# Performance work log

Measured on AMD Instinct MI355X. Metric: run time of the kernel, lower is better.

The kernel has to match this reference:

```python
import jax, jax.numpy as jnp
import numpy as np

N_NODES = 40000
N_EDGES = 640000
IN, HID, OUT = 128, 256, 47


def setup_inputs() -> dict:
    key = jax.random.key(0)
    ks = jax.random.split(key, 8)
    x = jax.random.normal(ks[0], (N_NODES, IN), dtype=jnp.float32)
    # PyTorch Linear(fan_in, fan_out): store as [fan_in, fan_out] for y = h @ W + b
    W1 = jax.random.normal(ks[1], (2 * IN, HID), dtype=jnp.float32) / np.sqrt(2 * IN)
    b1 = jnp.zeros((HID,), jnp.float32)
    W2 = jax.random.normal(ks[2], (2 * HID, HID), dtype=jnp.float32) / np.sqrt(2 * HID)
    b2 = jnp.zeros((HID,), jnp.float32)
    W3 = jax.random.normal(ks[3], (2 * HID, OUT), dtype=jnp.float32) / np.sqrt(2 * HID)
    b3 = jnp.zeros((OUT,), jnp.float32)
    src = jax.random.randint(ks[4], (N_EDGES,), 0, N_NODES, dtype=jnp.int64 if jax.config.jax_enable_x64 else jnp.int32)
    dst = jax.random.randint(ks[5], (N_EDGES,), 0, N_NODES, dtype=jnp.int64 if jax.config.jax_enable_x64 else jnp.int32)
    return {"x": x, "W1": W1, "b1": b1, "W2": W2, "b2": b2, "W3": W3, "b3": b3,
            "src": src, "dst": dst}


def _sage_layer(h, src, dst, W, b):
    # copy_u -> mean: gather src features, scatter-sum into dst, divide by in-degree
    msum = jax.ops.segment_sum(h[src], dst, num_segments=N_NODES)  # [N, d]
    deg = jax.ops.segment_sum(jnp.ones_like(dst, dtype=h.dtype), dst, num_segments=N_NODES)
    mean = msum / jnp.maximum(deg, 1.0)[:, None]  # zero-degree nodes get 0 (DGL mean convention)
    cat = jnp.concatenate([h, mean], axis=1)      # [N, 2d]
    return cat @ W + b


def reference(x, W1, b1, W2, b2, W3, b3, src, dst):
    # dropout is identity in eval mode
    h = jax.nn.relu(_sage_layer(x, src, dst, W1, b1))
    h = jax.nn.relu(_sage_layer(h, src, dst, W2, b2))
    return _sage_layer(h, src, dst, W3, b3)
```

## Files before the change

kernel.cpp:

```cpp
#include <hip/hip_runtime.h>

#define NNODES 40000
#define NEDGES 640000
#define DIN 128
#define DHID 256
#define DOUT 47
#define NCNT 40960
#define NPART (NCNT / 256)

typedef __attribute__((ext_vector_type(8))) short short8;
typedef __attribute__((ext_vector_type(4))) float f32x4;

__device__ inline float bf2f(unsigned short u) {
    union { unsigned int i; float f; } c; c.i = ((unsigned int)u) << 16; return c.f;
}
__device__ inline unsigned short f2bf(float f) {
    union { float f; unsigned int i; } c; c.f = f;
    unsigned int x = c.i;
    x += 0x7fff + ((x >> 16) & 1);
    return (unsigned short)(x >> 16);
}

__global__ void hist_kernel(const int* __restrict__ dst, int* __restrict__ cnt) {
    int t = blockIdx.x * blockDim.x + threadIdx.x;
    if (t < NEDGES) atomicAdd(&cnt[dst[t]], 1);
}

__global__ void part_kernel(const int* __restrict__ cnt, int* __restrict__ part) {
    int b = blockIdx.x, t = threadIdx.x;
    int v = cnt[b * 256 + t];
#pragma unroll
    for (int off = 32; off > 0; off >>= 1) v += __shfl_down(v, off);
    __shared__ int ws[4];
    if ((t & 63) == 0) ws[t >> 6] = v;
    __syncthreads();
    if (t == 0) part[b] = ws[0] + ws[1] + ws[2] + ws[3];
}

__global__ void scanpart_kernel(const int* __restrict__ part, int* __restrict__ partoff) {
    __shared__ int sh[256];
    int t = threadIdx.x;
    int v = (t < NPART) ? part[t] : 0;
    sh[t] = v;
    __syncthreads();
    for (int off = 1; off < 256; off <<= 1) {
        int add = (t >= off) ? sh[t - off] : 0;
        __syncthreads();
        sh[t] += add;
        __syncthreads();
    }
    if (t < NPART) partoff[t] = sh[t] - v;
}

__global__ void writeptr_kernel(const int* __restrict__ cnt, const int* __restrict__ partoff,
                                int* __restrict__ rowptr) {
    __shared__ int sh[256];
    int b = blockIdx.x, t = threadIdx.x;
    int idx = b * 256 + t;
    int v = cnt[idx];
    sh[t] = v;
    __syncthreads();
    for (int off = 1; off < 256; off <<= 1) {
        int add = (t >= off) ? sh[t - off] : 0;
        __syncthreads();
        sh[t] += add;
        __syncthreads();
    }
    rowptr[idx] = partoff[b] + sh[t] - v;
}

__global__ void fill_kernel(const int* __restrict__ src, const int* __restrict__ dst,
                            const int* __restrict__ rowptr, int* __restrict__ fill,
                            unsigned short* __restrict__ eidx) {
    int e = blockIdx.x * blockDim.x + threadIdx.x;
    if (e < NEDGES) {
        int d = dst[e];
        int pos = rowptr[d] + atomicAdd(&fill[d], 1);
        eidx[pos] = (unsigned short)src[e];
    }
}

__global__ void f32_to_bf16x4_kernel(const float4* __restrict__ in, ushort4* __restrict__ out, int n4) {
    int t = blockIdx.x * blockDim.x + threadIdx.x;
    if (t < n4) {
        float4 v = in[t];
        ushort4 r;
        r.x = f2bf(v.x); r.y = f2bf(v.y); r.z = f2bf(v.z); r.w = f2bf(v.w);
        out[t] = r;
    }
}

__global__ void conv_wt_kernel(const float* __restrict__ W, unsigned short* __restrict__ Wt, int K, int N) {
    int t = blockIdx.x * blockDim.x + threadIdx.x;
    if (t < K * N) {
        int k = t / N, n = t - k * N;
        Wt[(size_t)n * K + k] = f2bf(W[t]);
    }
}

__global__ void conv_wt3_kernel(const float* __restrict__ W3, unsigned short* __restrict__ Wt) {
    int t = blockIdx.x * blockDim.x + threadIdx.x;
    if (t < 94 * 256) {
        int n = t >> 8, k = t & 255;
        float v = (n < 47) ? W3[(size_t)k * DOUT + n]
                           : W3[(size_t)(k + DHID) * DOUT + (n - 47)];
        Wt[t] = f2bf(v);
    }
}

template <int D>
__global__ void agg_bf16_kernel(const unsigned short* __restrict__ h,
                                const int* __restrict__ rowptr,
                                const unsigned short* __restrict__ eidx,
                                unsigned short* __restrict__ mean) {
    constexpr int VPL = D / 64;
    const int node = blockIdx.x * (blockDim.x >> 6) + (threadIdx.x >> 6);
    if (node >= NNODES) return;
    const int lane = threadIdx.x & 63;
    const int beg = rowptr[node], end = rowptr[node + 1];
    const unsigned short* hp = h + lane * VPL;

    float acc[VPL];
#pragma unroll
    for (int i = 0; i < VPL; ++i) acc[i] = 0.0f;

    for (int base = beg; base < end; base += 64) {
        int n = min(64, end - base);
        int myidx = (base + lane < end) ? (int)eidx[base + lane] : 0;
        int j = 0;
        for (; j + 8 <= n; j += 8) {
            int s[8];
#pragma unroll
            for (int u = 0; u < 8; ++u) s[u] = __shfl(myidx, j + u);
            if constexpr (VPL == 4) {
                ushort4 v[8];
#pragma unroll
                for (int u = 0; u < 8; ++u) v[u] = *(const ushort4*)(hp + (size_t)s[u] * D);
#pragma unroll
                for (int u = 0; u < 8; ++u) {
                    acc[0] += bf2f(v[u].x); acc[1] += bf2f(v[u].y);
                    acc[2] += bf2f(v[u].z); acc[3] += bf2f(v[u].w);
                }
            } else {
                ushort2 v[8];
#pragma unroll
                for (int u = 0; u < 8; ++u) v[u] = *(const ushort2*)(hp + (size_t)s[u] * D);
#pragma unroll
                for (int u = 0; u < 8; ++u) {
                    acc[0] += bf2f(v[u].x); acc[1] += bf2f(v[u].y);
                }
            }
        }
        for (; j + 4 <= n; j += 4) {
            int s[4];
#pragma unroll
            for (int u = 0; u < 4; ++u) s[u] = __shfl(myidx, j + u);
            if constexpr (VPL == 4) {
                ushort4 v[4];
#pragma unroll
                for (int u = 0; u < 4; ++u) v[u] = *(const ushort4*)(hp + (size_t)s[u] * D);
#pragma unroll
                for (int u = 0; u < 4; ++u) {
                    acc[0] += bf2f(v[u].x); acc[1] += bf2f(v[u].y);
                    acc[2] += bf2f(v[u].z); acc[3] += bf2f(v[u].w);
                }
            } else {
                ushort2 v[4];
#pragma unroll
                for (int u = 0; u < 4; ++u) v[u] = *(const ushort2*)(hp + (size_t)s[u] * D);
#pragma unroll
                for (int u = 0; u < 4; ++u) {
                    acc[0] += bf2f(v[u].x); acc[1] += bf2f(v[u].y);
                }
            }
        }
        for (; j < n; ++j) {
            int s = __shfl(myidx, j);
            if constexpr (VPL == 4) {
                ushort4 v = *(const ushort4*)(hp + (size_t)s * D);
                acc[0] += bf2f(v.x); acc[1] += bf2f(v.y);
                acc[2] += bf2f(v.z); acc[3] += bf2f(v.w);
            } else {
                ushort2 v = *(const ushort2*)(hp + (size_t)s * D);
                acc[0] += bf2f(v.x); acc[1] += bf2f(v.y);
            }
        }
    }
    float inv = (end > beg) ? 1.0f / (float)(end - beg) : 0.0f;
    unsigned short* o = mean + (size_t)node * D + lane * VPL;
    if constexpr (VPL == 4) {
        ushort4 r;
        r.x = f2bf(acc[0] * inv); r.y = f2bf(acc[1] * inv);
        r.z = f2bf(acc[2] * inv); r.w = f2bf(acc[3] * inv);
        *(ushort4*)o = r;
    } else {
        ushort2 r;
        r.x = f2bf(acc[0] * inv); r.y = f2bf(acc[1] * inv);
        *(ushort2*)o = r;
    }
}

__global__ void agg_p_kernel(const unsigned short* __restrict__ P,
                             const int* __restrict__ rowptr,
                             const unsigned short* __restrict__ eidx,
                             float* __restrict__ out) {
    const int node = blockIdx.x * (blockDim.x >> 6) + (threadIdx.x >> 6);
    if (node >= NNODES) return;
    const int lane = threadIdx.x & 63;
    const int beg = rowptr[node], end = rowptr[node + 1];
    const bool active = lane < 48;
    const int lc = active ? lane : 0;

    float acc = 0.0f;
    for (int base = beg; base < end; base += 64) {
        int n = min(64, end - base);
        int myidx = (base + lane < end) ? (int)eidx[base + lane] : 0;
        int j = 0;
        for (; j + 4 <= n; j += 4) {
            int s0 = __shfl(myidx, j);
            int s1 = __shfl(myidx, j + 1);
            int s2 = __shfl(myidx, j + 2);
            int s3 = __shfl(myidx, j + 3);
            if (active) {
                float a = bf2f(P[(size_t)s0 * 48 + lc]) + bf2f(P[(size_t)s1 * 48 + lc]);
                float b = bf2f(P[(size_t)s2 * 48 + lc]) + bf2f(P[(size_t)s3 * 48 + lc]);
                acc += a + b;
            }
        }
        for (; j < n; ++j) {
            int s = __shfl(myidx, j);
            if (active) acc += bf2f(P[(size_t)s * 48 + lc]);
        }
    }
    if (lane < 47 && end > beg) {
        out[(size_t)node * DOUT + lane] += acc / (float)(end - beg);
    }
}

template <int MODE>
__launch_bounds__(256, 2)
__global__ void gemm_mfma_kernel(const unsigned short* __restrict__ H,
                                 const unsigned short* __restrict__ Mn,
                                 const unsigned short* __restrict__ Wt,
                                 const float* __restrict__ bias,
                                 void* __restrict__ outp,
                                 unsigned short* __restrict__ Pout,
                                 int d, int N) {
    const int K = 2 * d;
    __shared__ uint4 AsB[128 * 4];
    __shared__ uint4 BsB[128 * 4];

    const int tid = threadIdx.x;
    const int lane = tid & 63;
    const int wid = tid >> 6;
    const int wr = wid >> 1, wc = wid & 1;
    const int row0 = blockIdx.x * 128;
    const int col0 = blockIdx.y * 128;

    const int sr = tid >> 1;
    const int sh = tid & 1;
    const int gar = min(row0 + sr, NNODES - 1);
    const int gbr = min(col0 + sr, N - 1);
    const int ssw = (sr >> 1) & 3;

    f32x4 acc[4][4];
#pragma unroll
    for (int m = 0; m < 4; ++m)
#pragma unroll
        for (int n = 0; n < 4; ++n) {
            f32x4 z = {0.0f, 0.0f, 0.0f, 0.0f};
            acc[m][n] = z;
        }

    for (int k0 = 0; k0 < K; k0 += 32) {
        {
            int kb = k0 + sh * 16;
            const unsigned short* p;
            if (MODE == 2) {
                p = H + (size_t)gar * K + kb;
            } else {
                p = (kb < d) ? (H + (size_t)gar * d + kb)
                             : (Mn + (size_t)gar * d + (kb - d));
            }
            uint4 v0 = *(const uint4*)p;
            uint4 v1 = *(const uint4*)(p + 8);
            AsB[sr * 4 + ((2 * sh) ^ ssw)]     = v0;
            AsB[sr * 4 + ((2 * sh + 1) ^ ssw)] = v1;
        }
        {
            const unsigned short* p = Wt + (size_t)gbr * K + k0 + sh * 16;
            uint4 v0 = *(const uint4*)p;
            uint4 v1 = *(const uint4*)(p + 8);
            BsB[sr * 4 + ((2 * sh) ^ ssw)]     = v0;
            BsB[sr * 4 + ((2 * sh + 1) ^ ssw)] = v1;
        }
        __syncthreads();

        short8 af[4], bfr[4];
        const int fr = lane & 15;
        const int slot = lane >> 4;
#pragma unroll
        for (int m = 0; m < 4; ++m) {
            int r = wr * 64 + m * 16 + fr;
            union { uint4 u; short8 s; } cc;
            cc.u = AsB[r * 4 + (slot ^ ((r >> 1) & 3))];
            af[m] = cc.s;
        }
#pragma unroll
        for (int n = 0; n < 4; ++n) {
            int r = wc * 64 + n * 16 + fr;
            union { uint4 u; short8 s; } cc;
            cc.u = BsB[r * 4 + (slot ^ ((r >> 1) & 3))];
            bfr[n] = cc.s;
        }
#pragma unroll
        for (int m = 0; m < 4; ++m)
#pragma unroll
            for (int n = 0; n < 4; ++n)
                acc[m][n] = __builtin_amdgcn_mfma_f32_16x16x32_bf16(af[m], bfr[n], acc[m][n], 0, 0, 0);
        __syncthreads();
    }

#pragma unroll
    for (int m = 0; m < 4; ++m) {
#pragma unroll
        for (int n = 0; n < 4; ++n) {
            int col = col0 + wc * 64 + n * 16 + (lane & 15);
            if (col >= N) continue;
            float bv = (MODE == 0) ? bias[col] : ((col < 47) ? bias[col] : 0.0f);
#pragma unroll
            for (int q = 0; q < 4; ++q) {
                int row = row0 + wr * 64 + m * 16 + (lane >> 4) * 4 + q;
                if (row < NNODES) {
                    float v = acc[m][n][q] + bv;
                    if (MODE == 0) {
                        v = fmaxf(v, 0.0f);
                        ((unsigned short*)outp)[(size_t)row * N + col] = f2bf(v);
                    } else {
                        if (col < 47) ((float*)outp)[(size_t)row * DOUT + col] = v;
                        else Pout[(size_t)row * 48 + (col - 47)] = f2bf(v);
                    }
                }
            }
        }
    }
}

extern "C" void kernel_launch(void* const* d_in, const int* in_sizes, int n_in,
                              void* d_out, int out_size, void* d_ws, size_t ws_size,
                              hipStream_t stream) {
    const float* x  = (const float*)d_in[0];
    const float* W1 = (const float*)d_in[1];
    const float* b1 = (const float*)d_in[2];
    const float* W2 = (const float*)d_in[3];
    const float* b2 = (const float*)d_in[4];
    const float* W3 = (const float*)d_in[5];
    const float* b3 = (const float*)d_in[6];
    const int* src  = (const int*)d_in[7];
    const int* dst  = (const int*)d_in[8];
    float* out = (float*)d_out;

    int* rowptr  = (int*)d_ws;
    unsigned short* eidx = (unsigned short*)(rowptr + NCNT);
    int* cnt     = (int*)(eidx + NEDGES);
    int* fill    = cnt + NCNT;
    int* part    = fill + NCNT;
    int* partoff = part + 256;
    unsigned short* xbf  = (unsigned short*)(partoff + 256);
    unsigned short* h1   = xbf + (size_t)NNODES * DIN;
    unsigned short* h2   = h1 + (size_t)NNODES * DHID;
    unsigned short* mean = h2 + (size_t)NNODES * DHID;
    unsigned short* wt1  = mean + (size_t)NNODES * DHID;
    unsigned short* wt2  = wt1 + 2 * DIN * DHID;
    unsigned short* wt3  = wt2 + 2 * DHID * DHID;
    unsigned short* P    = mean;

    hipMemsetAsync(cnt, 0, 2 * NCNT * sizeof(int), stream);
    hist_kernel<<<(NEDGES + 255) / 256, 256, 0, stream>>>(dst, cnt);
    part_kernel<<<NPART, 256, 0, stream>>>(cnt, part);
    scanpart_kernel<<<1, 256, 0, stream>>>(part, partoff);
    writeptr_kernel<<<NPART, 256, 0, stream>>>(cnt, partoff, rowptr);
    fill_kernel<<<(NEDGES + 255) / 256, 256, 0, stream>>>(src, dst, rowptr, fill, eidx);

    f32_to_bf16x4_kernel<<<(NNODES * DIN / 4 + 255) / 256, 256, 0, stream>>>(
        (const float4*)x, (ushort4*)xbf, NNODES * DIN / 4);
    conv_wt_kernel<<<(2 * DIN * DHID + 255) / 256, 256, 0, stream>>>(W1, wt1, 2 * DIN, DHID);
    conv_wt_kernel<<<(2 * DHID * DHID + 255) / 256, 256, 0, stream>>>(W2, wt2, 2 * DHID, DHID);
    conv_wt3_kernel<<<(94 * 256 + 255) / 256, 256, 0, stream>>>(W3, wt3);

    const int MB = (NNODES + 127) / 128;

    agg_bf16_kernel<DIN><<<NNODES / 4, 256, 0, stream>>>(xbf, rowptr, eidx, mean);
    {
        dim3 grid(MB, 2);
        gemm_mfma_kernel<0><<<grid, 256, 0, stream>>>(xbf, mean, wt1, b1, h1, nullptr, DIN, DHID);
    }

    agg_bf16_kernel<DHID><<<NNODES / 4, 256, 0, stream>>>(h1, rowptr, eidx, mean);
    {
        dim3 grid(MB, 2);
        gemm_mfma_kernel<0><<<grid, 256, 0, stream>>>(h1, mean, wt2, b2, h2, nullptr, DHID, DHID);
    }

    {
        dim3 grid(MB, 1);
        gemm_mfma_kernel<2><<<grid, 256, 0, stream>>>(h2, h2, wt3, b3, out, P, DHID / 2, 94);
    }
    agg_p_kernel<<<NNODES / 4, 256, 0, stream>>>(P, rowptr, eidx, out);
}
```

Baseline: 236.3 us.

## Fuse neighbor mean aggregation into layer GEMM via shared-memory mean tile

Layers 1 and 2 now run one fused kernel per 64-node tile. Each wave first gathers and averages neighbor features for 16 nodes into a swizzled LDS tile, then the block runs the MFMA GEMM over the concatenation of h (read from global) and the LDS mean, with the full 256 output columns per block. This drops the global write and re-read of the mean buffer and two kernel launches per layer. The costs are far fewer blocks (625), a serial per-wave gather phase before compute with no overlap, and a larger LDS footprint that may lower occupancy.

New measurement: 324.1 us. 37.1% more time.

```diff
diff --git a/kernel.cpp b/kernel.cpp
--- a/kernel.cpp
+++ b/kernel.cpp
@@ -109,94 +109,160 @@
 }
 
 template <int D>
-__global__ void agg_bf16_kernel(const unsigned short* __restrict__ h,
-                                const int* __restrict__ rowptr,
-                                const unsigned short* __restrict__ eidx,
-                                unsigned short* __restrict__ mean) {
+__launch_bounds__(256, 2)
+__global__ void fused_layer_kernel(const unsigned short* __restrict__ h,
+                                   const int* __restrict__ rowptr,
+                                   const unsigned short* __restrict__ eidx,
+                                   const unsigned short* __restrict__ Wt,
+                                   const float* __restrict__ bias,
+                                   unsigned short* __restrict__ hout) {
+    constexpr int K = 2 * D;
     constexpr int VPL = D / 64;
-    const int node = blockIdx.x * (blockDim.x >> 6) + (threadIdx.x >> 6);
-    if (node >= NNODES) return;
-    const int lane = threadIdx.x & 63;
-    const int beg = rowptr[node], end = rowptr[node + 1];
-    const unsigned short* hp = h + lane * VPL;
-
-    float acc[VPL];
-#pragma unroll
-    for (int i = 0; i < VPL; ++i) acc[i] = 0.0f;
-
-    for (int base = beg; base < end; base += 64) {
-        int n = min(64, end - base);
-        int myidx = (base + lane < end) ? (int)eidx[base + lane] : 0;
-        int j = 0;
-        for (; j + 8 <= n; j += 8) {
-            int s[8];
-#pragma unroll
-            for (int u = 0; u < 8; ++u) s[u] = __shfl(myidx, j + u);
+    constexpr int SLOTS = D / 8;
+    __shared__ uint4 meanS[64 * SLOTS];
+    __shared__ uint4 As[64 * 4];
+    __shared__ uint4 Bs[256 * 4];
+
+    const int tid = threadIdx.x;
+    const int lane = tid & 63;
+    const int w = tid >> 6;
+    const int row0 = blockIdx.x * 64;
+
+    {
+        uint* ms = (uint*)meanS;
+        const unsigned short* hp = h + lane * VPL;
+        for (int i = 0; i < 16; ++i) {
+            const int r = w * 16 + i;
+            const int node = row0 + r;
+            const int beg = rowptr[node], end = rowptr[node + 1];
+            float acc[VPL];
+#pragma unroll
+            for (int q = 0; q < VPL; ++q) acc[q] = 0.0f;
+            for (int base = beg; base < end; base += 64) {
+                int n = min(64, end - base);
+                int myidx = (base + lane < end) ? (int)eidx[base + lane] : 0;
+                int j = 0;
+                for (; j + 4 <= n; j += 4) {
+                    int s0 = __shfl(myidx, j);
+                    int s1 = __shfl(myidx, j + 1);
+                    int s2 = __shfl(myidx, j + 2);
+                    int s3 = __shfl(myidx, j + 3);
+                    if constexpr (VPL == 4) {
+                        ushort4 v0 = *(const ushort4*)(hp + (size_t)s0 * D);
+                        ushort4 v1 = *(const ushort4*)(hp + (size_t)s1 * D);
+                        ushort4 v2 = *(const ushort4*)(hp + (size_t)s2 * D);
+                        ushort4 v3 = *(const ushort4*)(hp + (size_t)s3 * D);
+                        acc[0] += (bf2f(v0.x) + bf2f(v1.x)) + (bf2f(v2.x) + bf2f(v3.x));
+                        acc[1] += (bf2f(v0.y) + bf2f(v1.y)) + (bf2f(v2.y) + bf2f(v3.y));
+                        acc[2] += (bf2f(v0.z) + bf2f(v1.z)) + (bf2f(v2.z) + bf2f(v3.z));
+                        acc[3] += (bf2f(v0.w) + bf2f(v1.w)) + (bf2f(v2.w) + bf2f(v3.w));
+                    } else {
+                        ushort2 v0 = *(const ushort2*)(hp + (size_t)s0 * D);
+                        ushort2 v1 = *(const ushort2*)(hp + (size_t)s1 * D);
+                        ushort2 v2 = *(const ushort2*)(hp + (size_t)s2 * D);
+                        ushort2 v3 = *(const ushort2*)(hp + (size_t)s3 * D);
+                        acc[0] += (bf2f(v0.x) + bf2f(v1.x)) + (bf2f(v2.x) + bf2f(v3.x));
+                        acc[1] += (bf2f(v0.y) + bf2f(v1.y)) + (bf2f(v2.y) + bf2f(v3.y));
+                    }
+                }
+                for (; j < n; ++j) {
+                    int s = __shfl(myidx, j);
+                    if constexpr (VPL == 4) {
+                        ushort4 v = *(const ushort4*)(hp + (size_t)s * D);
+                        acc[0] += bf2f(v.x); acc[1] += bf2f(v.y);
+                        acc[2] += bf2f(v.z); acc[3] += bf2f(v.w);
+                    } else {
+                        ushort2 v = *(const ushort2*)(hp + (size_t)s * D);
+                        acc[0] += bf2f(v.x); acc[1] += bf2f(v.y);
+                    }
+                }
+            }
+            float inv = (end > beg) ? 1.0f / (float)(end - beg) : 0.0f;
             if constexpr (VPL == 4) {
-                ushort4 v[8];
-#pragma unroll
-                for (int u = 0; u < 8; ++u) v[u] = *(const ushort4*)(hp + (size_t)s[u] * D);
-#pragma unroll
-                for (int u = 0; u < 8; ++u) {
-                    acc[0] += bf2f(v[u].x); acc[1] += bf2f(v[u].y);
-                    acc[2] += bf2f(v[u].z); acc[3] += bf2f(v[u].w);
-                }
+                uint lo = (uint)f2bf(acc[0] * inv) | ((uint)f2bf(acc[1] * inv) << 16);
+                uint hi = (uint)f2bf(acc[2] * inv) | ((uint)f2bf(acc[3] * inv) << 16);
+                int sw = (lane >> 1) ^ (r & 7);
+                int bi = r * (D / 2) + sw * 4 + (lane & 1) * 2;
+                ms[bi] = lo;
+                ms[bi + 1] = hi;
             } else {
-                ushort2 v[8];
-#pragma unroll
-                for (int u = 0; u < 8; ++u) v[u] = *(const ushort2*)(hp + (size_t)s[u] * D);
-#pragma unroll
-                for (int u = 0; u < 8; ++u) {
-                    acc[0] += bf2f(v[u].x); acc[1] += bf2f(v[u].y);
-                }
-            }
-        }
-        for (; j + 4 <= n; j += 4) {
-            int s[4];
-#pragma unroll
-            for (int u = 0; u < 4; ++u) s[u] = __shfl(myidx, j + u);
-            if constexpr (VPL == 4) {
-                ushort4 v[4];
-#pragma unroll
-                for (int u = 0; u < 4; ++u) v[u] = *(const ushort4*)(hp + (size_t)s[u] * D);
-#pragma unroll
-                for (int u = 0; u < 4; ++u) {
-                    acc[0] += bf2f(v[u].x); acc[1] += bf2f(v[u].y);
-                    acc[2] += bf2f(v[u].z); acc[3] += bf2f(v[u].w);
-                }
+                uint lo = (uint)f2bf(acc[0] * inv) | ((uint)f2bf(acc[1] * inv) << 16);
+                int sw = (lane >> 2) ^ (r & 7);
+                ms[r * (D / 2) + sw * 4 + (lane & 3)] = lo;
+            }
+        }
+    }
+    __syncthreads();
+
+    f32x4 acc[4][4];
+#pragma unroll
+    for (int m = 0; m < 4; ++m)
+#pragma unroll
+        for (int n = 0; n < 4; ++n) {
+            f32x4 z = {0.0f, 0.0f, 0.0f, 0.0f};
+            acc[m][n] = z;
+        }
+
+    const int fr = lane & 15;
+    const int sl = lane >> 4;
+    const int sar = tid >> 2;
+    const int sak = tid & 3;
+
+#pragma unroll
+    for (int k0 = 0; k0 < K; k0 += 32) {
+        if (k0 < D) {
+            As[sar * 4 + (sak ^ ((sar >> 1) & 3))] =
+                *(const uint4*)(h + (size_t)(row0 + sar) * D + k0 + sak * 8);
+        }
+        {
+            const unsigned short* p = Wt + (size_t)tid * K + k0;
+#pragma unroll
+            for (int s = 0; s < 4; ++s)
+                Bs[tid * 4 + (s ^ ((tid >> 1) & 3))] = *(const uint4*)(p + s * 8);
+        }
+        __syncthreads();
+
+        short8 af[4], bfv[4];
+#pragma unroll
+        for (int m = 0; m < 4; ++m) {
+            int r = m * 16 + fr;
+            union { uint4 u; short8 s; } cc;
+            if (k0 < D) {
+                cc.u = As[r * 4 + (sl ^ ((r >> 1) & 3))];
             } else {
-                ushort2 v[4];
-#pragma unroll
-                for (int u = 0; u < 4; ++u) v[u] = *(const ushort2*)(hp + (size_t)s[u] * D);
-#pragma unroll
-                for (int u = 0; u < 4; ++u) {
-                    acc[0] += bf2f(v[u].x); acc[1] += bf2f(v[u].y);
-                }
-            }
-        }
-        for (; j < n; ++j) {
-            int s = __shfl(myidx, j);
-            if constexpr (VPL == 4) {
-                ushort4 v = *(const ushort4*)(hp + (size_t)s * D);
-                acc[0] += bf2f(v.x); acc[1] += bf2f(v.y);
-                acc[2] += bf2f(v.z); acc[3] += bf2f(v.w);
-            } else {
-                ushort2 v = *(const ushort2*)(hp + (size_t)s * D);
-                acc[0] += bf2f(v.x); acc[1] += bf2f(v.y);
-            }
-        }
-    }
-    float inv = (end > beg) ? 1.0f / (float)(end - beg) : 0.0f;
-    unsigned short* o = mean + (size_t)node * D + lane * VPL;
-    if constexpr (VPL == 4) {
-        ushort4 r;
-        r.x = f2bf(acc[0] * inv); r.y = f2bf(acc[1] * inv);
-        r.z = f2bf(acc[2] * inv); r.w = f2bf(acc[3] * inv);
-        *(ushort4*)o = r;
-    } else {
-        ushort2 r;
-        r.x = f2bf(acc[0] * inv); r.y = f2bf(acc[1] * inv);
-        *(ushort2*)o = r;
+                int s = ((k0 - D) >> 3) + sl;
+                cc.u = meanS[r * SLOTS + (s ^ (r & 7))];
+            }
+            af[m] = cc.s;
+        }
+#pragma unroll
+        for (int n = 0; n < 4; ++n) {
+            int r = w * 64 + n * 16 + fr;
+            union { uint4 u; short8 s; } cc;
+            cc.u = Bs[r * 4 + (sl ^ ((r >> 1) & 3))];
+            bfv[n] = cc.s;
+        }
+#pragma unroll
+        for (int m = 0; m < 4; ++m)
+#pragma unroll
+            for (int n = 0; n < 4; ++n)
+                acc[m][n] = __builtin_amdgcn_mfma_f32_16x16x32_bf16(af[m], bfv[n], acc[m][n], 0, 0, 0);
+        __syncthreads();
+    }
+
+#pragma unroll
+    for (int m = 0; m < 4; ++m) {
+#pragma unroll
+        for (int n = 0; n < 4; ++n) {
+            int col = w * 64 + n * 16 + fr;
+            float bv = bias[col];
+#pragma unroll
+            for (int q = 0; q < 4; ++q) {
+                int row = row0 + m * 16 + sl * 4 + q;
+                float v = fmaxf(acc[m][n][q] + bv, 0.0f);
+                hout[(size_t)row * 256 + col] = f2bf(v);
+            }
+        }
     }
 }
 
@@ -237,15 +303,13 @@
     }
 }
 
-template <int MODE>
 __launch_bounds__(256, 2)
-__global__ void gemm_mfma_kernel(const unsigned short* __restrict__ H,
-                                 const unsigned short* __restrict__ Mn,
-                                 const unsigned short* __restrict__ Wt,
-                                 const float* __restrict__ bias,
-                                 void* __restrict__ outp,
-                                 unsigned short* __restrict__ Pout,
-                                 int d, int N) {
+__global__ void gemm3_kernel(const unsigned short* __restrict__ H,
+                             const unsigned short* __restrict__ Wt,
+                             const float* __restrict__ bias,
+                             float* __restrict__ outp,
+                             unsigned short* __restrict__ Pout,
+                             int d, int N) {
     const int K = 2 * d;
     __shared__ uint4 AsB[128 * 4];
     __shared__ uint4 BsB[128 * 4];
@@ -255,12 +319,11 @@
     const int wid = tid >> 6;
     const int wr = wid >> 1, wc = wid & 1;
     const int row0 = blockIdx.x * 128;
-    const int col0 = blockIdx.y * 128;
 
     const int sr = tid >> 1;
     const int sh = tid & 1;
     const int gar = min(row0 + sr, NNODES - 1);
-    const int gbr = min(col0 + sr, N - 1);
+    const int gbr = min(sr, N - 1);
     const int ssw = (sr >> 1) & 3;
 
     f32x4 acc[4][4];
@@ -274,14 +337,7 @@
 
     for (int k0 = 0; k0 < K; k0 += 32) {
         {
-            int kb = k0 + sh * 16;
-            const unsigned short* p;
-            if (MODE == 2) {
-                p = H + (size_t)gar * K + kb;
-            } else {
-                p = (kb < d) ? (H + (size_t)gar * d + kb)
-                             : (Mn + (size_t)gar * d + (kb - d));
-            }
+            const unsigned short* p = H + (size_t)gar * K + k0 + sh * 16;
             uint4 v0 = *(const uint4*)p;
             uint4 v1 = *(const uint4*)(p + 8);
             AsB[sr * 4 + ((2 * sh) ^ ssw)]     = v0;
@@ -296,7 +352,7 @@
         }
         __syncthreads();
 
-        short8 af[4], bfr[4];
+        short8 af[4], bfv[4];
         const int fr = lane & 15;
         const int slot = lane >> 4;
 #pragma unroll
@@ -311,13 +367,13 @@
             int r = wc * 64 + n * 16 + fr;
             union { uint4 u; short8 s; } cc;
             cc.u = BsB[r * 4 + (slot ^ ((r >> 1) & 3))];
-            bfr[n] = cc.s;
+            bfv[n] = cc.s;
         }
 #pragma unroll
         for (int m = 0; m < 4; ++m)
 #pragma unroll
             for (int n = 0; n < 4; ++n)
-                acc[m][n] = __builtin_amdgcn_mfma_f32_16x16x32_bf16(af[m], bfr[n], acc[m][n], 0, 0, 0);
+                acc[m][n] = __builtin_amdgcn_mfma_f32_16x16x32_bf16(af[m], bfv[n], acc[m][n], 0, 0, 0);
         __syncthreads();
     }
 
@@ -325,21 +381,16 @@
     for (int m = 0; m < 4; ++m) {
 #pragma unroll
         for (int n = 0; n < 4; ++n) {
-            int col = col0 + wc * 64 + n * 16 + (lane & 15);
+            int col = wc * 64 + n * 16 + (lane & 15);
             if (col >= N) continue;
-            float bv = (MODE == 0) ? bias[col] : ((col < 47) ? bias[col] : 0.0f);
+            float bv = (col < 47) ? bias[col] : 0.0f;
 #pragma unroll
             for (int q = 0; q < 4; ++q) {
                 int row = row0 + wr * 64 + m * 16 + (lane >> 4) * 4 + q;
                 if (row < NNODES) {
                     float v = acc[m][n][q] + bv;
-                    if (MODE == 0) {
-                        v = fmaxf(v, 0.0f);
-                        ((unsigned short*)outp)[(size_t)row * N + col] = f2bf(v);
-                    } else {
-                        if (col < 47) ((float*)outp)[(size_t)row * DOUT + col] = v;
-                        else Pout[(size_t)row * 48 + (col - 47)] = f2bf(v);
-                    }
+                    if (col < 47) outp[(size_t)row * DOUT + col] = v;
+                    else Pout[(size_t)row * 48 + (col - 47)] = f2bf(v);
                 }
             }
         }
@@ -369,11 +420,10 @@
     unsigned short* xbf  = (unsigned short*)(partoff + 256);
     unsigned short* h1   = xbf + (size_t)NNODES * DIN;
     unsigned short* h2   = h1 + (size_t)NNODES * DHID;
-    unsigned short* mean = h2 + (size_t)NNODES * DHID;
-    unsigned short* wt1  = mean + (size_t)NNODES * DHID;
+    unsigned short* P    = h2 + (size_t)NNODES * DHID;
+    unsigned short* wt1  = P + (size_t)NNODES * 48;
     unsigned short* wt2  = wt1 + 2 * DIN * DHID;
     unsigned short* wt3  = wt2 + 2 * DHID * DHID;
-    unsigned short* P    = mean;
 
     hipMemsetAsync(cnt, 0, 2 * NCNT * sizeof(int), stream);
     hist_kernel<<<(NEDGES + 255) / 256, 256, 0, stream>>>(dst, cnt);
@@ -388,23 +438,10 @@
     conv_wt_kernel<<<(2 * DHID * DHID + 255) / 256, 256, 0, stream>>>(W2, wt2, 2 * DHID, DHID);
     conv_wt3_kernel<<<(94 * 256 + 255) / 256, 256, 0, stream>>>(W3, wt3);
 
-    const int MB = (NNODES + 127) / 128;
-
-    agg_bf16_kernel<DIN><<<NNODES / 4, 256, 0, stream>>>(xbf, rowptr, eidx, mean);
-    {
-        dim3 grid(MB, 2);
-        gemm_mfma_kernel<0><<<grid, 256, 0, stream>>>(xbf, mean, wt1, b1, h1, nullptr, DIN, DHID);
-    }
-
-    agg_bf16_kernel<DHID><<<NNODES / 4, 256, 0, stream>>>(h1, rowptr, eidx, mean);
-    {
-        dim3 grid(MB, 2);
-        gemm_mfma_kernel<0><<<grid, 256, 0, stream>>>(h1, mean, wt2, b2, h2, nullptr, DHID, DHID);
-    }
-
-    {
-        dim3 grid(MB, 1);
-        gemm_mfma_kernel<2><<<grid, 256, 0, stream>>>(h2, h2, wt3, b3, out, P, DHID / 2, 94);
-    }
+    fused_layer_kernel<DIN><<<NNODES / 64, 256, 0, stream>>>(xbf, rowptr, eidx, wt1, b1, h1);
+
+    fused_layer_kernel<DHID><<<NNODES / 64, 256, 0, stream>>>(h1, rowptr, eidx, wt2, b2, h2);
+
+    gemm3_kernel<<<(NNODES + 127) / 128, 256, 0, stream>>>(h2, wt3, b3, out, P, DHID / 2, 94);
     agg_p_kernel<<<NNODES / 4, 256, 0, stream>>>(P, rowptr, eidx, out);
 }
```

## Use direct global-to-LDS loads in full-width layer GEMMs and merge conversion kernels

Applied to the files above, without the earlier changes.

The layer-1/2 GEMMs now use 64-row tiles that cover all 256 output columns in one block, so the A tile is read once instead of being reloaded for two column blocks. Tiles are staged through global_load_lds (direct global-to-LDS transfers), with the swizzle applied on the global address side so no VGPRs are needed for staging. The four input and weight conversion kernels are merged into one launch to cut launch overhead. Risks include a larger B tile in LDS per block, no bounds checks (this relies on NNODES dividing by 64), and a fully unrolled k loop that raises code size.

New measurement: 219.2 us. 1.08x faster.

```diff
diff --git a/kernel.cpp b/kernel.cpp
--- a/kernel.cpp
+++ b/kernel.cpp
@@ -10,6 +10,11 @@
 
 typedef __attribute__((ext_vector_type(8))) short short8;
 typedef __attribute__((ext_vector_type(4))) float f32x4;
+
+#define GLD16(gp, lp)                                                        \
+    __builtin_amdgcn_global_load_lds(                                        \
+        (const __attribute__((address_space(1))) void*)(gp),                 \
+        (__attribute__((address_space(3))) void*)(lp), 16, 0, 0)
 
 __device__ inline float bf2f(unsigned short u) {
     union { unsigned int i; float f; } c; c.i = ((unsigned int)u) << 16; return c.f;
@@ -80,31 +85,38 @@
     }
 }
 
-__global__ void f32_to_bf16x4_kernel(const float4* __restrict__ in, ushort4* __restrict__ out, int n4) {
+__global__ void conv_all_kernel(const float* __restrict__ x,
+                                const float* __restrict__ W1,
+                                const float* __restrict__ W2,
+                                const float* __restrict__ W3,
+                                unsigned short* __restrict__ xbf,
+                                unsigned short* __restrict__ wt1,
+                                unsigned short* __restrict__ wt2,
+                                unsigned short* __restrict__ wt3) {
+    const int N0 = NNODES * DIN / 4;
+    const int N1 = 2 * DIN * DHID;
+    const int N2 = 2 * DHID * DHID;
+    const int N3 = 94 * 256;
     int t = blockIdx.x * blockDim.x + threadIdx.x;
-    if (t < n4) {
-        float4 v = in[t];
+    if (t < N0) {
+        float4 v = ((const float4*)x)[t];
         ushort4 r;
         r.x = f2bf(v.x); r.y = f2bf(v.y); r.z = f2bf(v.z); r.w = f2bf(v.w);
-        out[t] = r;
-    }
-}
-
-__global__ void conv_wt_kernel(const float* __restrict__ W, unsigned short* __restrict__ Wt, int K, int N) {
-    int t = blockIdx.x * blockDim.x + threadIdx.x;
-    if (t < K * N) {
-        int k = t / N, n = t - k * N;
-        Wt[(size_t)n * K + k] = f2bf(W[t]);
-    }
-}
-
-__global__ void conv_wt3_kernel(const float* __restrict__ W3, unsigned short* __restrict__ Wt) {
-    int t = blockIdx.x * blockDim.x + threadIdx.x;
-    if (t < 94 * 256) {
-        int n = t >> 8, k = t & 255;
+        ((ushort4*)xbf)[t] = r;
+    } else if (t < N0 + N1) {
+        int u = t - N0;
+        int k = u >> 8, n = u & 255;
+        wt1[(size_t)n * 256 + k] = f2bf(W1[u]);
+    } else if (t < N0 + N1 + N2) {
+        int u = t - N0 - N1;
+        int k = u >> 8, n = u & 255;
+        wt2[(size_t)n * 512 + k] = f2bf(W2[u]);
+    } else if (t < N0 + N1 + N2 + N3) {
+        int u = t - N0 - N1 - N2;
+        int n = u >> 8, k = u & 255;
         float v = (n < 47) ? W3[(size_t)k * DOUT + n]
                            : W3[(size_t)(k + DHID) * DOUT + (n - 47)];
-        Wt[t] = f2bf(v);
+        wt3[u] = f2bf(v);
     }
 }
 
@@ -237,15 +249,103 @@
     }
 }
 
-template <int MODE>
+template <int D>
 __launch_bounds__(256, 2)
-__global__ void gemm_mfma_kernel(const unsigned short* __restrict__ H,
-                                 const unsigned short* __restrict__ Mn,
-                                 const unsigned short* __restrict__ Wt,
-                                 const float* __restrict__ bias,
-                                 void* __restrict__ outp,
-                                 unsigned short* __restrict__ Pout,
-                                 int d, int N) {
+__global__ void gemm_fused_kernel(const unsigned short* __restrict__ H,
+                                  const unsigned short* __restrict__ Mn,
+                                  const unsigned short* __restrict__ Wt,
+                                  const float* __restrict__ bias,
+                                  unsigned short* __restrict__ hout) {
+    constexpr int K = 2 * D;
+    __shared__ uint4 As4[64 * 4];
+    __shared__ uint4 Bs4[256 * 4];
+
+    const int tid = threadIdx.x;
+    const int lane = tid & 63;
+    const int w = tid >> 6;
+    const int row0 = blockIdx.x * 64;
+
+    const int lr = lane >> 2;
+    const int lslot = lane & 3;
+    const int arow = w * 16 + lr;
+    const int aoff = (lslot ^ ((arow >> 1) & 3)) * 8;
+    const size_t abase = (size_t)(row0 + arow) * D;
+
+    f32x4 acc[4][4];
+#pragma unroll
+    for (int m = 0; m < 4; ++m)
+#pragma unroll
+        for (int n = 0; n < 4; ++n) {
+            f32x4 z = {0.0f, 0.0f, 0.0f, 0.0f};
+            acc[m][n] = z;
+        }
+
+    const int fr = lane & 15;
+    const int sl = lane >> 4;
+
+#pragma unroll
+    for (int k0 = 0; k0 < K; k0 += 32) {
+        {
+            const unsigned short* ap = (k0 < D) ? (H + abase + k0 + aoff)
+                                                : (Mn + abase + (k0 - D) + aoff);
+            GLD16(ap, (char*)As4 + w * 1024);
+        }
+#pragma unroll
+        for (int c = 0; c < 4; ++c) {
+            int q = w * 4 + c;
+            int brow = q * 16 + lr;
+            const unsigned short* bp =
+                Wt + (size_t)brow * K + k0 + ((lslot ^ ((brow >> 1) & 3)) * 8);
+            GLD16(bp, (char*)Bs4 + q * 1024);
+        }
+        __syncthreads();
+
+        short8 af[4], bfv[4];
+#pragma unroll
+        for (int m = 0; m < 4; ++m) {
+            int r = m * 16 + fr;
+            union { uint4 u; short8 s; } cc;
+            cc.u = As4[r * 4 + (sl ^ ((r >> 1) & 3))];
+            af[m] = cc.s;
+        }
+#pragma unroll
+        for (int n = 0; n < 4; ++n) {
+            int r = w * 64 + n * 16 + fr;
+            union { uint4 u; short8 s; } cc;
+            cc.u = Bs4[r * 4 + (sl ^ ((r >> 1) & 3))];
+            bfv[n] = cc.s;
+        }
+#pragma unroll
+        for (int m = 0; m < 4; ++m)
+#pragma unroll
+            for (int n = 0; n < 4; ++n)
+                acc[m][n] = __builtin_amdgcn_mfma_f32_16x16x32_bf16(af[m], bfv[n], acc[m][n], 0, 0, 0);
+        __syncthreads();
+    }
+
+#pragma unroll
+    for (int m = 0; m < 4; ++m) {
+#pragma unroll
+        for (int n = 0; n < 4; ++n) {
+            int col = w * 64 + n * 16 + fr;
+            float bv = bias[col];
+#pragma unroll
+            for (int q = 0; q < 4; ++q) {
+                int row = row0 + m * 16 + sl * 4 + q;
+                float v = fmaxf(acc[m][n][q] + bv, 0.0f);
+                hout[(size_t)row * 256 + col] = f2bf(v);
+            }
+        }
+    }
+}
+
+__launch_bounds__(256, 2)
+__global__ void gemm3_kernel(const unsigned short* __restrict__ H,
+                             const unsigned short* __restrict__ Wt,
+                             const float* __restrict__ bias,
+                             float* __restrict__ outp,
+                             unsigned short* __restrict__ Pout,
+                             int d, int N) {
     const int K = 2 * d;
     __shared__ uint4 AsB[128 * 4];
     __shared__ uint4 BsB[128 * 4];
@@ -255,12 +355,11 @@
     const int wid = tid >> 6;
     const int wr = wid >> 1, wc = wid & 1;
     const int row0 = blockIdx.x * 128;
-    const int col0 = blockIdx.y * 128;
 
     const int sr = tid >> 1;
     const int sh = tid & 1;
     const int gar = min(row0 + sr, NNODES - 1);
-    const int gbr = min(col0 + sr, N - 1);
+    const int gbr = min(sr, N - 1);
     const int ssw = (sr >> 1) & 3;
 
     f32x4 acc[4][4];
@@ -274,14 +373,7 @@
 
     for (int k0 = 0; k0 < K; k0 += 32) {
         {
-            int kb = k0 + sh * 16;
-            const unsigned short* p;
-            if (MODE == 2) {
-                p = H + (size_t)gar * K + kb;
-            } else {
-                p = (kb < d) ? (H + (size_t)gar * d + kb)
-                             : (Mn + (size_t)gar * d + (kb - d));
-            }
+            const unsigned short* p = H + (size_t)gar * K + k0 + sh * 16;
             uint4 v0 = *(const uint4*)p;
             uint4 v1 = *(const uint4*)(p + 8);
             AsB[sr * 4 + ((2 * sh) ^ ssw)]     = v0;
@@ -296,7 +388,7 @@
         }
         __syncthreads();
 
-        short8 af[4], bfr[4];
+        short8 af[4], bfv[4];
         const int fr = lane & 15;
         const int slot = lane >> 4;
 #pragma unroll
@@ -311,13 +403,13 @@
             int r = wc * 64 + n * 16 + fr;
             union { uint4 u; short8 s; } cc;
             cc.u = BsB[r * 4 + (slot ^ ((r >> 1) & 3))];
-            bfr[n] = cc.s;
+            bfv[n] = cc.s;
         }
 #pragma unroll
         for (int m = 0; m < 4; ++m)
 #pragma unroll
             for (int n = 0; n < 4; ++n)
-                acc[m][n] = __builtin_amdgcn_mfma_f32_16x16x32_bf16(af[m], bfr[n], acc[m][n], 0, 0, 0);
+                acc[m][n] = __builtin_amdgcn_mfma_f32_16x16x32_bf16(af[m], bfv[n], acc[m][n], 0, 0, 0);
         __syncthreads();
     }
 
@@ -325,21 +417,16 @@
     for (int m = 0; m < 4; ++m) {
 #pragma unroll
         for (int n = 0; n < 4; ++n) {
-            int col = col0 + wc * 64 + n * 16 + (lane & 15);
+            int col = wc * 64 + n * 16 + (lane & 15);
             if (col >= N) continue;
-            float bv = (MODE == 0) ? bias[col] : ((col < 47) ? bias[col] : 0.0f);
+            float bv = (col < 47) ? bias[col] : 0.0f;
 #pragma unroll
             for (int q = 0; q < 4; ++q) {
                 int row = row0 + wr * 64 + m * 16 + (lane >> 4) * 4 + q;
                 if (row < NNODES) {
                     float v = acc[m][n][q] + bv;
-                    if (MODE == 0) {
-                        v = fmaxf(v, 0.0f);
-                        ((unsigned short*)outp)[(size_t)row * N + col] = f2bf(v);
-                    } else {
-                        if (col < 47) ((float*)outp)[(size_t)row * DOUT + col] = v;
-                        else Pout[(size_t)row * 48 + (col - 47)] = f2bf(v);
-                    }
+                    if (col < 47) outp[(size_t)row * DOUT + col] = v;
+                    else Pout[(size_t)row * 48 + (col - 47)] = f2bf(v);
                 }
             }
         }
@@ -382,29 +469,17 @@
     writeptr_kernel<<<NPART, 256, 0, stream>>>(cnt, partoff, rowptr);
     fill_kernel<<<(NEDGES + 255) / 256, 256, 0, stream>>>(src, dst, rowptr, fill, eidx);
 
-    f32_to_bf16x4_kernel<<<(NNODES * DIN / 4 + 255) / 256, 256, 0, stream>>>(
-        (const float4*)x, (ushort4*)xbf, NNODES * DIN / 4);
-    conv_wt_kernel<<<(2 * DIN * DHID + 255) / 256, 256, 0, stream>>>(W1, wt1, 2 * DIN, DHID);
-    conv_wt_kernel<<<(2 * DHID * DHID + 255) / 256, 256, 0, stream>>>(W2, wt2, 2 * DHID, DHID);
-    conv_wt3_kernel<<<(94 * 256 + 255) / 256, 256, 0, stream>>>(W3, wt3);
-
-    const int MB = (NNODES + 127) / 128;
+    {
+        const int NT = NNODES * DIN / 4 + 2 * DIN * DHID + 2 * DHID * DHID + 94 * 256;
+        conv_all_kernel<<<(NT + 255) / 256, 256, 0, stream>>>(x, W1, W2, W3, xbf, wt1, wt2, wt3);
+    }
 
     agg_bf16_kernel<DIN><<<NNODES / 4, 256, 0, stream>>>(xbf, rowptr, eidx, mean);
-    {
-        dim3 grid(MB, 2);
-        gemm_mfma_kernel<0><<<grid, 256, 0, stream>>>(xbf, mean, wt1, b1, h1, nullptr, DIN, DHID);
-    }
+    gemm_fused_kernel<DIN><<<NNODES / 64, 256, 0, stream>>>(xbf, mean, wt1, b1, h1);
 
     agg_bf16_kernel<DHID><<<NNODES / 4, 256, 0, stream>>>(h1, rowptr, eidx, mean);
-    {
-        dim3 grid(MB, 2);
-        gemm_mfma_kernel<0><<<grid, 256, 0, stream>>>(h1, mean, wt2, b2, h2, nullptr, DHID, DHID);
-    }
-
-    {
-        dim3 grid(MB, 1);
-        gemm_mfma_kernel<2><<<grid, 256, 0, stream>>>(h2, h2, wt3, b3, out, P, DHID / 2, 94);
-    }
+    gemm_fused_kernel<DHID><<<NNODES / 64, 256, 0, stream>>>(h1, mean, wt2, b2, h2);
+
+    gemm3_kernel<<<(NNODES + 127) / 128, 256, 0, stream>>>(h2, wt3, b3, out, P, DHID / 2, 94);
     agg_p_kernel<<<NNODES / 4, 256, 0, stream>>>(P, rowptr, eidx, out);
 }
```
